# Kernel tuning notes

Hardware: AMD Instinct MI355X
Metric: run time of the kernel (lower is better)

Reference implementation:

```python
import jax, jax.numpy as jnp
import numpy as np
from jax import lax

V, D, H, K, B, T = 32000, 300, 300, 9, 64, 512


def _lstm_dir(x, w_ih, w_hh, b_ih, b_hh, h0, c0):
    # x: [B, T, D]; torch gate order: i, f, g, o
    def step(carry, xt):
        h, c = carry
        gates = xt @ w_ih.T + h @ w_hh.T + b_ih + b_hh  # [B, 4H]
        i, f, g, o = jnp.split(gates, 4, axis=-1)
        i, f, o = jax.nn.sigmoid(i), jax.nn.sigmoid(f), jax.nn.sigmoid(o)
        g = jnp.tanh(g)
        c = f * c + i * g
        h = o * jnp.tanh(c)
        return (h, c), h

    xs = jnp.transpose(x, (1, 0, 2))  # [T, B, D]
    _, hs = lax.scan(step, (h0, c0), xs)
    return jnp.transpose(hs, (1, 0, 2))  # [B, T, H]


def _emissions(tokens, emb, w_ih_f, w_hh_f, b_ih_f, b_hh_f,
               w_ih_b, w_hh_b, b_ih_b, b_hh_b, h0, c0, w_out, b_out):
    x = emb[tokens]  # [B, T, D]
    hf = _lstm_dir(x, w_ih_f, w_hh_f, b_ih_f, b_hh_f, h0[0], c0[0])
    hb = _lstm_dir(jnp.flip(x, axis=1), w_ih_b, w_hh_b, b_ih_b, b_hh_b, h0[1], c0[1])
    hb = jnp.flip(hb, axis=1)
    out = jnp.concatenate([hf, hb], axis=-1)  # [B, T, 2H]
    return out @ w_out.T + b_out  # [B, T, K]


def _crf_nll(emissions, tags, mask, start_t, end_t, trans):
    # torchcrf: -sum_b log p(tags | emissions)
    e = jnp.transpose(emissions, (1, 0, 2))  # [T, B, K]
    tg = tags.T                               # [T, B]
    m = mask.T.astype(emissions.dtype)        # [T, B]
    bidx = jnp.arange(tags.shape[0])
    # numerator: gold path score
    num = start_t[tg[0]] + e[0][bidx, tg[0]]
    def nstep(carry, inp):
        et, tt, tp, mt = inp
        return carry + (trans[tp, tt] + et[bidx, tt]) * mt, None
    num, _ = lax.scan(nstep, num, (e[1:], tg[1:], tg[:-1], m[1:]))
    last_idx = mask.sum(axis=1).astype(jnp.int32) - 1
    last_tags = tags[bidx, last_idx]
    num = num + end_t[last_tags]
    # denominator: forward algorithm
    alpha = start_t + e[0]  # [B, K]
    def dstep(alpha, inp):
        et, mt = inp
        nxt = jax.scipy.special.logsumexp(alpha[:, :, None] + trans[None], axis=1) + et
        return jnp.where(mt[:, None] > 0, nxt, alpha), None
    alpha, _ = lax.scan(dstep, alpha, (e[1:], m[1:]))
    den = jax.scipy.special.logsumexp(alpha + end_t, axis=1)
    return -jnp.sum(num - den)


def _viterbi(emissions, mask, start_t, end_t, trans):
    e = jnp.transpose(emissions, (1, 0, 2))  # [T, B, K]
    m = mask.T                               # [T, B]
    score = start_t + e[0]                   # [B, K]
    def fstep(score, inp):
        et, mt = inp
        br = score[:, :, None] + trans[None]  # [B, K_prev, K_next]
        best = br.max(axis=1)
        idx = br.argmax(axis=1).astype(jnp.int32)  # [B, K]
        new = best + et
        return jnp.where(mt[:, None], new, score), idx
    score, history = lax.scan(fstep, score, (e[1:], m[1:]))  # history: [T-1, B, K]
    score = score + end_t
    last = jnp.argmax(score, axis=-1).astype(jnp.int32)  # [B]
    def bstep(tag, inp):
        idx_t, mt = inp
        prev = jnp.take_along_axis(idx_t, tag[:, None], axis=1)[:, 0]
        tag = jnp.where(mt, prev, tag)
        return tag, tag
    _, tags_rev = lax.scan(bstep, last, (history, m[1:]), reverse=True)  # [T-1, B]
    path = jnp.concatenate([tags_rev, last[None]], axis=0)  # [T, B]
    return path.T  # [B, T]


def setup_inputs() -> dict:
    key = jax.random.key(0)
    ks = jax.random.split(key, 20)
    s = 0.1
    emb = jax.random.normal(ks[0], (V, D), jnp.float32) * s
    emb = emb.at[0].set(0.0)  # padding_idx row
    inp = {
        "tokens": jax.random.randint(ks[1], (B, T), 0, V, jnp.int32),
        "tags": jax.random.randint(ks[2], (B, T), 0, K, jnp.int32),
        "mask": jnp.ones((B, T), jnp.bool_),
        "emb": emb,
        "w_ih_f": jax.random.normal(ks[3], (4 * H, D), jnp.float32) * s,
        "w_hh_f": jax.random.normal(ks[4], (4 * H, H), jnp.float32) * s,
        "b_ih_f": jax.random.normal(ks[5], (4 * H,), jnp.float32) * s,
        "b_hh_f": jax.random.normal(ks[6], (4 * H,), jnp.float32) * s,
        "w_ih_b": jax.random.normal(ks[7], (4 * H, D), jnp.float32) * s,
        "w_hh_b": jax.random.normal(ks[8], (4 * H, H), jnp.float32) * s,
        "b_ih_b": jax.random.normal(ks[9], (4 * H,), jnp.float32) * s,
        "b_hh_b": jax.random.normal(ks[10], (4 * H,), jnp.float32) * s,
        "h0": jax.random.normal(ks[11], (2, B, H), jnp.float32),
        "c0": jax.random.normal(ks[12], (2, B, H), jnp.float32),
        "w_out": jax.random.normal(ks[13], (K, 2 * H), jnp.float32) * s,
        "b_out": jax.random.normal(ks[14], (K,), jnp.float32) * s,
        "start_t": jax.random.normal(ks[15], (K,), jnp.float32) * s,
        "end_t": jax.random.normal(ks[16], (K,), jnp.float32) * s,
        "trans": jax.random.normal(ks[17], (K, K), jnp.float32) * s,
    }
    return inp


def reference(tokens, tags, mask, emb, w_ih_f, w_hh_f, b_ih_f, b_hh_f,
              w_ih_b, w_hh_b, b_ih_b, b_hh_b, h0, c0, w_out, b_out,
              start_t, end_t, trans):
    feats = _emissions(tokens, emb, w_ih_f, w_hh_f, b_ih_f, b_hh_f,
                       w_ih_b, w_hh_b, b_ih_b, b_hh_b, h0, c0, w_out, b_out)
    paths = _viterbi(feats, mask, start_t, end_t, trans)
    loss = _crf_nll(feats, tags, mask, start_t, end_t, trans)
    return paths, loss
```

## Files before the change

kernel.cpp:

```cpp
#include <hip/hip_runtime.h>
#include <math.h>

#define NV 32000
#define ND 300
#define NH 300
#define NK 9
#define NB 64
#define NT 512

typedef short bf16x8 __attribute__((ext_vector_type(8)));
typedef float f32x4  __attribute__((ext_vector_type(4)));

__device__ inline short bf16r(float x) {
    return (short)((__float_as_uint(x) + 0x8000u) >> 16);
}

__device__ inline float tanh_fast(float x) {
    float e2 = __expf(2.f * x);
    return 1.f - 2.f / (e2 + 1.f);
}

__device__ inline void bar_lds() {
    asm volatile("s_waitcnt lgkmcnt(0)" ::: "memory");
    __builtin_amdgcn_s_barrier();
    asm volatile("" ::: "memory");
}

#define WB_OFF   0ull
#define WB_F     768000ull
#define E_OFF    (WB_OFF + WB_F)
#define E_SZ     ((unsigned long long)NT*NB*NK)
#define CBUF_OFF (E_OFF + E_SZ)
#define CBUF_SZ  (2ull*NB*NH)
#define HSLOT_OFF (CBUF_OFF + CBUF_SZ)
#define HSLOT_SZ  (2ull*2*NB*NH)
#define XP_OFF   (HSLOT_OFF + HSLOT_SZ)
#define XPC_SZ   (2ull*64*1200*64)

__global__ __launch_bounds__(256) void k_wcvt(
    const float* __restrict__ wihf, const float* __restrict__ wihb,
    const float* __restrict__ whhf, const float* __restrict__ whhb,
    short* __restrict__ dst)
{
    int i = blockIdx.x*256 + threadIdx.x;
    if (i >= 1536000) return;
    int d  = i / 384000;
    int r2 = i % 384000;
    int j  = r2 / 320, k = r2 % 320;
    const float* src = (d == 0) ? wihf : (d == 1) ? wihb : (d == 2) ? whhf : whhb;
    float v = (k < 300) ? src[(size_t)j*300 + k] : 0.f;
    dst[i] = bf16r(v);
}

__global__ __launch_bounds__(256) void k_xproj(
    const int* __restrict__ tokens, const float* __restrict__ emb,
    const short* __restrict__ wb16,
    const float* __restrict__ bif, const float* __restrict__ bhf,
    const float* __restrict__ bib, const float* __restrict__ bhb,
    float* __restrict__ xpc, int chunk)
{
    const int tid = threadIdx.x;
    const int w  = tid >> 6, L = tid & 63;
    const int lm = L & 15, lq = L >> 4;
    const int dir = blockIdx.z;
    const int m0 = blockIdx.x*128 + w*32;
    const int n0 = blockIdx.y*80;
    const int tbase = dir ? (448 - chunk*64) : (chunk*64);

    const float* arow[2];
#pragma unroll
    for (int mi = 0; mi < 2; ++mi) {
        int m = m0 + mi*16 + lm;
        int b = m >> 6, lt = m & 63;
        arow[mi] = emb + (size_t)tokens[b*512 + tbase + lt] * 300;
    }
    const short* brow[5];
#pragma unroll
    for (int ni = 0; ni < 5; ++ni) {
        int j = n0 + ni*16 + lm;
        brow[ni] = wb16 + ((size_t)dir*1200 + j)*320;
    }

    f32x4 acc[2][5];
#pragma unroll
    for (int mi = 0; mi < 2; ++mi)
#pragma unroll
        for (int ni = 0; ni < 5; ++ni)
#pragma unroll
            for (int r = 0; r < 4; ++r) acc[mi][ni][r] = 0.f;

    const float4 z4 = make_float4(0.f,0.f,0.f,0.f);
    for (int k0 = 0; k0 < 320; k0 += 32) {
        const int kk = k0 + lq*8;
        bf16x8 af[2], bf[5];
#pragma unroll
        for (int mi = 0; mi < 2; ++mi) {
            float4 f1 = (kk   < 300) ? *(const float4*)(arow[mi] + kk)     : z4;
            float4 f2 = (kk+4 < 300) ? *(const float4*)(arow[mi] + kk + 4) : z4;
            af[mi][0]=bf16r(f1.x); af[mi][1]=bf16r(f1.y); af[mi][2]=bf16r(f1.z); af[mi][3]=bf16r(f1.w);
            af[mi][4]=bf16r(f2.x); af[mi][5]=bf16r(f2.y); af[mi][6]=bf16r(f2.z); af[mi][7]=bf16r(f2.w);
        }
#pragma unroll
        for (int ni = 0; ni < 5; ++ni)
            bf[ni] = *(const bf16x8*)(brow[ni] + kk);
#pragma unroll
        for (int mi = 0; mi < 2; ++mi)
#pragma unroll
            for (int ni = 0; ni < 5; ++ni)
                acc[mi][ni] = __builtin_amdgcn_mfma_f32_16x16x32_bf16(
                                  af[mi], bf[ni], acc[mi][ni], 0, 0, 0);
    }

#pragma unroll
    for (int ni = 0; ni < 5; ++ni) {
        int j = n0 + ni*16 + lm;
        int g = j/300, rr = j%300;
        int slc = rr/20, ul = rr%20;
        float bias = dir ? (bib[j]+bhb[j]) : (bif[j]+bhf[j]);
#pragma unroll
        for (int mi = 0; mi < 2; ++mi) {
#pragma unroll
            for (int r = 0; r < 4; ++r) {
                int m = m0 + mi*16 + lq*4 + r;
                int b = m >> 6, lt = m & 63;
                int sp = dir ? (63 - lt) : lt;
                size_t idx = ((((size_t)dir*64 + sp)*8 + (b>>3))*15 + slc)*640
                           + (size_t)(b&7)*80 + g*20 + ul;
                xpc[idx] = acc[mi][ni][r] + bias;
            }
        }
    }
}

__global__ __launch_bounds__(256) void k_rnn(
    const float* __restrict__ xpc,
    const short* __restrict__ whh16,
    const float* __restrict__ h0,
    unsigned* hslot, float* __restrict__ cbuf,
    float* __restrict__ ev, const float* __restrict__ wout,
    int s_begin, int s_count, int full)
{
    extern __shared__ char lds_pad[];
    __shared__ __align__(16) short h_sh16[16*328];
    __shared__ __align__(16) float xp_sh[640];
    __shared__ __align__(16) float gates_sh[80*9];
    __shared__ __align__(16) float wo_sh[180];
    __shared__ __align__(16) float hloc[160];
    __shared__ __align__(16) float ev_loc[64*72];
    (void)lds_pad;

    const int tid = threadIdx.x;
    const int wv  = tid >> 6, L = tid & 63;
    const int lm  = L & 15, lq = L >> 4;
    const int dir = blockIdx.x / 120;
    const int rem = blockIdx.x % 120;
    const int sl  = rem / 8;
    const int gb  = rem % 8;
    const int u0  = sl * 20;

    const int tb = (wv == 0) ? 0 : (wv + 1);
    const int tn = (wv == 0) ? 2 : 1;

    bf16x8 A[2][10];
#pragma unroll 2
    for (int mt = 0; mt < 2; ++mt) {
        if (mt < tn) {
            int r = (tb + mt)*16 + lm;
            int grow = (r/20)*300 + u0 + (r%20);
            const short* wr = whh16 + ((size_t)dir*1200 + grow)*320;
#pragma unroll
            for (int ks = 0; ks < 10; ++ks)
                A[mt][ks] = *(const bf16x8*)(wr + ks*32 + lq*8);
        }
    }
    if (tid < 180) wo_sh[tid] = wout[(tid/20)*600 + dir*300 + u0 + (tid%20)];

    for (int i = tid; i < 16*328; i += 256) h_sh16[i] = 0;

    const bool isPW = (tid < 160);
    const int bl_p = tid/20, lu_p = tid%20;
    float c_reg = 0.f;
    if (isPW) c_reg = cbuf[((size_t)dir*NB + gb*8 + bl_p)*NH + u0 + lu_p];

    auto xaddr = [&](int s) -> const float* {
        const float* xb; int sp;
        if (full) { xb = xpc + (size_t)(s >> 6)*XPC_SZ; sp = s & 63; }
        else      { xb = xpc;                            sp = s - s_begin; }
        return xb + ((((size_t)dir*64 + sp)*8 + gb)*15 + sl)*640 + (size_t)tid*4;
    };
    float4 xpr;
    if (tid < 160) xpr = *(const float4*)xaddr(s_begin);

    bar_lds();

    for (int s = s_begin; s < s_begin + s_count; ++s) {
        unsigned vb[10];
        unsigned* hsrc = hslot + (((size_t)(s & 1)*2 + dir)*NB + gb*8)*NH;
        if (s > 0 && tid < 240) {
#pragma unroll
            for (int j = 0; j < 10; ++j) {
                int i = tid + 256*j;
                if (i < 2400)
                    vb[j] = __hip_atomic_load(hsrc + i, __ATOMIC_RELAXED,
                                              __HIP_MEMORY_SCOPE_AGENT);
            }
        }

        if (tid < 160) *(float4*)(&xp_sh[tid*4]) = xpr;
        if (tid < 160 && (s + 1) < s_begin + s_count)
            xpr = *(const float4*)xaddr(s + 1);

        if (s == 0) {
            const float* h0p = h0 + ((size_t)dir*NB + gb*8)*NH;
            for (int i = tid; i < 2400; i += 256)
                h_sh16[(i/300)*328 + (i%300)] = bf16r(h0p[i]);
        } else if (tid < 240) {
            const unsigned tg = (unsigned)s & 0xFFFFu;
            bool ok = false;
            while (!ok) {
                ok = true;
#pragma unroll
                for (int j = 0; j < 10; ++j) {
                    int i = tid + 256*j;
                    if (i < 2400 && (vb[j] >> 16) != tg) {
                        ok = false;
                        vb[j] = __hip_atomic_load(hsrc + i, __ATOMIC_RELAXED,
                                                  __HIP_MEMORY_SCOPE_AGENT);
                    }
                }
            }
#pragma unroll
            for (int j = 0; j < 10; ++j) {
                int i = tid + 256*j;
                if (i < 2400)
                    h_sh16[(i/300)*328 + (i%300)] = (short)(vb[j] & 0xFFFFu);
            }
        }
        bar_lds();

        {
            bf16x8 Bf[10];
#pragma unroll
            for (int ks = 0; ks < 10; ++ks)
                Bf[ks] = *(const bf16x8*)(h_sh16 + lm*328 + ks*32 + lq*8);
            f32x4 acc0, acc1;
#pragma unroll 2
            for (int mt = 0; mt < 2; ++mt) {
                if (mt < tn) {
#pragma unroll
                    for (int r = 0; r < 4; ++r) { acc0[r] = 0.f; acc1[r] = 0.f; }
#pragma unroll
                    for (int ks = 0; ks < 5; ++ks)
                        acc0 = __builtin_amdgcn_mfma_f32_16x16x32_bf16(
                                   A[mt][ks], Bf[ks], acc0, 0, 0, 0);
#pragma unroll
                    for (int ks = 5; ks < 10; ++ks)
                        acc1 = __builtin_amdgcn_mfma_f32_16x16x32_bf16(
                                   A[mt][ks], Bf[ks], acc1, 0, 0, 0);
                    if (lm < 8) {
#pragma unroll
                        for (int r = 0; r < 4; ++r)
                            gates_sh[((tb+mt)*16 + lq*4 + r)*9 + lm] = acc0[r] + acc1[r];
                    }
                }
            }
        }
        bar_lds();

        if (isPW) {
            float G[4];
#pragma unroll
            for (int g = 0; g < 4; ++g)
                G[g] = xp_sh[bl_p*80 + g*20 + lu_p] + gates_sh[(g*20 + lu_p)*9 + bl_p];
            float ig = 1.f/(1.f+__expf(-G[0]));
            float fg = 1.f/(1.f+__expf(-G[1]));
            float gg = tanh_fast(G[2]);
            float og = 1.f/(1.f+__expf(-G[3]));
            c_reg = fg*c_reg + ig*gg;
            float h = og*tanh_fast(c_reg);
            unsigned hb = (__float_as_uint(h) + 0x8000u) >> 16;
            unsigned pk = (((unsigned)(s+1) & 0xFFFFu) << 16) | hb;
            __hip_atomic_store(
                &hslot[(((size_t)((s+1)&1)*2 + dir)*NB + gb*8 + bl_p)*NH + u0 + lu_p],
                pk, __ATOMIC_RELAXED, __HIP_MEMORY_SCOPE_AGENT);
            hloc[bl_p*20 + lu_p] = h;
        }
        bar_lds();

        const int widx = (s - s_begin) & 63;
        if (tid < 72) {
            int b = tid/9, k = tid%9;
            float a = 0.f;
#pragma unroll
            for (int u = 0; u < 20; ++u) a += hloc[b*20+u]*wo_sh[k*20+u];
            ev_loc[widx*72 + tid] = a;
        }

        if (widx == 63) {
            bar_lds();
            const int sbase = s - 63;
            for (int i = tid; i < 64*72; i += 256) {
                int wi = i / 72, j = i % 72;
                int bb = j / 9, kk = j % 9;
                int tt = dir ? (511 - (sbase + wi)) : (sbase + wi);
                atomicAdd(&ev[((size_t)tt*NB + gb*8 + bb)*NK + kk], ev_loc[i]);
            }
        }
    }

    if (isPW) cbuf[((size_t)dir*NB + gb*8 + bl_p)*NH + u0 + lu_p] = c_reg;
}

#define BT_C 14
#define BT_L 37

__global__ __launch_bounds__(128) void k_crf(
    const float* __restrict__ ev, const int* __restrict__ tags,
    const float* __restrict__ start_t, const float* __restrict__ end_t,
    const float* __restrict__ trans, const float* __restrict__ bout,
    float* __restrict__ out)
{
    __shared__ __align__(16) float ex_a[12];
    __shared__ __align__(16) float ex_v[12];
    __shared__ int hist_sh[511*NK];
    __shared__ int fmap[BT_C*NK];
    __shared__ int entry_sh[BT_C];
    __shared__ int last_sh;

    const int b = blockIdx.x, tid = threadIdx.x;
    const int wv = tid >> 6, ln = tid & 63;

    if (wv == 0) {
        float part = 0.f;
        for (int t = ln; t < NT; t += 64) {
            int tc = tags[b*NT + t];
            float e = ev[((size_t)t*NB + b)*NK + tc] + bout[tc];
            float pre = (t == 0) ? start_t[tc] : trans[tags[b*NT + t - 1]*9 + tc];
            part += pre + e;
        }
        if (ln == 63) part += end_t[tags[b*NT + NT - 1]];
#pragma unroll
        for (int off = 32; off > 0; off >>= 1)
            part += __shfl_down(part, off, 64);
        const float num = part;

        if (ln < 9) {
            const int kc = ln;
            float Tc[9];
#pragma unroll
            for (int kp = 0; kp < 9; ++kp) Tc[kp] = __expf(trans[kp*9 + kc]);
            const float bo = bout[kc];
            ex_a[kc] = start_t[kc] + ev[(size_t)b*NK + kc] + bo;
            float etn = ev[((size_t)1*NB + b)*NK + kc] + bo;

            for (int t = 1; t < NT; ++t) {
                float et = etn;
                if (t + 1 < NT) etn = ev[((size_t)(t+1)*NB + b)*NK + kc] + bo;

                float4 s0 = *(const float4*)(&ex_a[0]);
                float4 s1 = *(const float4*)(&ex_a[4]);
                float  a8 = ex_a[8];
                float a0=s0.x,a1=s0.y,a2=s0.z,a3=s0.w,a4=s1.x,a5=s1.y,a6=s1.z,a7=s1.w;

                float M = fmaxf(fmaxf(fmaxf(a0,a1),fmaxf(a2,a3)),
                                fmaxf(fmaxf(a4,a5),fmaxf(a6,a7)));
                M = fmaxf(M, a8);
                float s =        __expf(a0-M)*Tc[0];
                s = fmaf(__expf(a1-M), Tc[1], s);
                s = fmaf(__expf(a2-M), Tc[2], s);
                s = fmaf(__expf(a3-M), Tc[3], s);
                s = fmaf(__expf(a4-M), Tc[4], s);
                s = fmaf(__expf(a5-M), Tc[5], s);
                s = fmaf(__expf(a6-M), Tc[6], s);
                s = fmaf(__expf(a7-M), Tc[7], s);
                s = fmaf(__expf(a8-M), Tc[8], s);
                ex_a[kc] = M + __logf(s) + et;
            }

            if (ln == 0) {
                float M = -1e30f;
#pragma unroll
                for (int k = 0; k < 9; ++k) M = fmaxf(M, ex_a[k] + end_t[k]);
                float ls = 0.f;
#pragma unroll
                for (int k = 0; k < 9; ++k) ls += __expf(ex_a[k] + end_t[k] - M);
                float den = M + __logf(ls);
                atomicAdd(out + NB*NT, den - num);
            }
        }
    } else {
        if (ln < 9) {
            const int kc = ln;
            float Tc[9];
#pragma unroll
            for (int kp = 0; kp < 9; ++kp) Tc[kp] = trans[kp*9 + kc];
            const float bo = bout[kc];
            ex_v[kc] = start_t[kc] + ev[(size_t)b*NK + kc] + bo;
            float etn = ev[((size_t)1*NB + b)*NK + kc] + bo;

            for (int t = 1; t < NT; ++t) {
                float et = etn;
                if (t + 1 < NT) etn = ev[((size_t)(t+1)*NB + b)*NK + kc] + bo;

                float4 s0 = *(const float4*)(&ex_v[0]);
                float4 s1 = *(const float4*)(&ex_v[4]);
                float  a8 = ex_v[8];
                float a0=s0.x,a1=s0.y,a2=s0.z,a3=s0.w,a4=s1.x,a5=s1.y,a6=s1.z,a7=s1.w;

                float bv = a0 + Tc[0]; int arg = 0;
                float v;
                v = a1+Tc[1]; if (v > bv) { bv = v; arg = 1; }
                v = a2+Tc[2]; if (v > bv) { bv = v; arg = 2; }
                v = a3+Tc[3]; if (v > bv) { bv = v; arg = 3; }
                v = a4+Tc[4]; if (v > bv) { bv = v; arg = 4; }
                v = a5+Tc[5]; if (v > bv) { bv = v; arg = 5; }
                v = a6+Tc[6]; if (v > bv) { bv = v; arg = 6; }
                v = a7+Tc[7]; if (v > bv) { bv = v; arg = 7; }
                v = a8+Tc[8]; if (v > bv) { bv = v; arg = 8; }
                hist_sh[(t-1)*NK + kc] = arg;
                ex_v[kc] = bv + et;
            }

            if (ln == 0) {
                float best = -1e30f; int last = 0;
#pragma unroll
                for (int k = 0; k < 9; ++k) {
                    float v = ex_v[k] + end_t[k];
                    if (v > best) { best = v; last = k; }
                }
                last_sh = last;
            }
        }
    }

    __syncthreads();

    if (tid < BT_C*NK) {
        int c = tid / NK, s = tid % NK;
        int lo = c*BT_L, hi = min(511, lo + BT_L);
        int pos = s;
        for (int i = hi - 1; i >= lo; --i) pos = hist_sh[i*NK + pos];
        fmap[c*NK + s] = pos;
    }
    __syncthreads();
    if (tid == 0) {
        int e = last_sh;
        entry_sh[BT_C-1] = e;
        for (int c = BT_C - 2; c >= 0; --c) {
            e = fmap[(c+1)*NK + e];
            entry_sh[c] = e;
        }
    }
    __syncthreads();
    int* pout = (int*)out;
    if (tid < BT_C) {
        int c = tid;
        int lo = c*BT_L, hi = min(511, lo + BT_L);
        int pos = entry_sh[c];
        for (int i = hi - 1; i >= lo; --i) {
            pos = hist_sh[i*NK + pos];
            pout[b*NT + i] = pos;
        }
    }
    if (tid == 0) pout[b*NT + NT - 1] = last_sh;
}

extern "C" void kernel_launch(void* const* d_in, const int* in_sizes, int n_in,
                              void* d_out, int out_size, void* d_ws, size_t ws_size,
                              hipStream_t stream)
{
    (void)in_sizes; (void)n_in;

    const int*   tokens = (const int*)  d_in[0];
    const int*   tags   = (const int*)  d_in[1];
    const float* emb    = (const float*)d_in[3];
    const float* wihf   = (const float*)d_in[4];
    const float* whhf   = (const float*)d_in[5];
    const float* bihf   = (const float*)d_in[6];
    const float* bhhf   = (const float*)d_in[7];
    const float* wihb   = (const float*)d_in[8];
    const float* whhb   = (const float*)d_in[9];
    const float* bib    = (const float*)d_in[10];
    const float* bhhb   = (const float*)d_in[11];
    const float* h0     = (const float*)d_in[12];
    const float* c0     = (const float*)d_in[13];
    const float* wout   = (const float*)d_in[14];
    const float* bout   = (const float*)d_in[15];
    const float* startt = (const float*)d_in[16];
    const float* endt   = (const float*)d_in[17];
    const float* trans  = (const float*)d_in[18];

    float* ws    = (float*)d_ws;
    short* wb16  = (short*)(ws + WB_OFF);
    short* whh16 = wb16 + 768000;
    float* evp   = ws + E_OFF;
    float* cbuf  = ws + CBUF_OFF;
    unsigned* hslot = (unsigned*)(ws + HSLOT_OFF);
    float* xp    = ws + XP_OFF;
    float* out   = (float*)d_out;

    const size_t need_full = (XP_OFF + 8ull*XPC_SZ) * 4ull;
    const bool full = (ws_size >= need_full);

    (void)hipMemsetAsync(d_out, 0, (size_t)out_size * sizeof(float), stream);
    (void)hipMemsetAsync(evp, 0, (size_t)E_SZ * sizeof(float), stream);
    (void)hipMemcpyAsync(cbuf, c0, 2ull*NB*NH*sizeof(float), hipMemcpyDeviceToDevice, stream);

    k_wcvt<<<6000, 256, 0, stream>>>(wihf, wihb, whhf, whhb, wb16);

    if (full) {
        for (int c = 0; c < 8; ++c)
            k_xproj<<<dim3(32, 15, 2), 256, 0, stream>>>(
                tokens, emb, wb16, bihf, bhhf, bib, bhhb, xp + (size_t)c*XPC_SZ, c);
        k_rnn<<<240, 256, 81920, stream>>>(
            xp, whh16, h0, hslot, cbuf, evp, wout, 0, 512, 1);
    } else {
        for (int c = 0; c < 8; ++c) {
            k_xproj<<<dim3(32, 15, 2), 256, 0, stream>>>(
                tokens, emb, wb16, bihf, bhhf, bib, bhhb, xp, c);
            k_rnn<<<240, 256, 81920, stream>>>(
                xp, whh16, h0, hslot, cbuf, evp, wout, c*64, 64, 0);
        }
    }
    k_crf<<<64, 128, 0, stream>>>(evp, tags, startt, endt, trans, bout, out);
}
```

Before: 2.005 ms.

## Fuse input projection and recurrence into one kernel with chunked software pipelining

Merges the input-projection GEMM and the LSTM recurrence into a single kernel. Blocks 0-239 run the recurrence for a 32-step chunk while the remaining blocks compute the projection for the next chunk into a double buffer. This hides projection work behind the latency-bound recurrence and drops the large full-sequence projection buffer. In exchange there are 17 launches instead of 9, chunks are half as long so more per-chunk setup and launch overhead, and the recurrence blocks share the GPU with GEMM blocks, which can slow their spin-wait synchronization.

```diff
diff --git a/kernel.cpp b/kernel.cpp
--- a/kernel.cpp
+++ b/kernel.cpp
@@ -35,7 +35,7 @@
 #define HSLOT_OFF (CBUF_OFF + CBUF_SZ)
 #define HSLOT_SZ  (2ull*2*NB*NH)
 #define XP_OFF   (HSLOT_OFF + HSLOT_SZ)
-#define XPC_SZ   (2ull*64*1200*64)
+#define XPC32_SZ (2ull*32*1200*64)
 
 __global__ __launch_bounds__(256) void k_wcvt(
     const float* __restrict__ wihf, const float* __restrict__ wihb,
@@ -52,263 +52,264 @@
     dst[i] = bf16r(v);
 }
 
-__global__ __launch_bounds__(256) void k_xproj(
+__global__ __launch_bounds__(256) void k_fused(
     const int* __restrict__ tokens, const float* __restrict__ emb,
     const short* __restrict__ wb16,
     const float* __restrict__ bif, const float* __restrict__ bhf,
     const float* __restrict__ bib, const float* __restrict__ bhb,
-    float* __restrict__ xpc, int chunk)
-{
-    const int tid = threadIdx.x;
-    const int w  = tid >> 6, L = tid & 63;
-    const int lm = L & 15, lq = L >> 4;
-    const int dir = blockIdx.z;
-    const int m0 = blockIdx.x*128 + w*32;
-    const int n0 = blockIdx.y*80;
-    const int tbase = dir ? (448 - chunk*64) : (chunk*64);
-
-    const float* arow[2];
-#pragma unroll
-    for (int mi = 0; mi < 2; ++mi) {
-        int m = m0 + mi*16 + lm;
-        int b = m >> 6, lt = m & 63;
-        arow[mi] = emb + (size_t)tokens[b*512 + tbase + lt] * 300;
-    }
-    const short* brow[5];
-#pragma unroll
-    for (int ni = 0; ni < 5; ++ni) {
-        int j = n0 + ni*16 + lm;
-        brow[ni] = wb16 + ((size_t)dir*1200 + j)*320;
-    }
-
-    f32x4 acc[2][5];
-#pragma unroll
-    for (int mi = 0; mi < 2; ++mi)
-#pragma unroll
-        for (int ni = 0; ni < 5; ++ni)
-#pragma unroll
-            for (int r = 0; r < 4; ++r) acc[mi][ni][r] = 0.f;
-
-    const float4 z4 = make_float4(0.f,0.f,0.f,0.f);
-    for (int k0 = 0; k0 < 320; k0 += 32) {
-        const int kk = k0 + lq*8;
-        bf16x8 af[2], bf[5];
-#pragma unroll
-        for (int mi = 0; mi < 2; ++mi) {
-            float4 f1 = (kk   < 300) ? *(const float4*)(arow[mi] + kk)     : z4;
-            float4 f2 = (kk+4 < 300) ? *(const float4*)(arow[mi] + kk + 4) : z4;
-            af[mi][0]=bf16r(f1.x); af[mi][1]=bf16r(f1.y); af[mi][2]=bf16r(f1.z); af[mi][3]=bf16r(f1.w);
-            af[mi][4]=bf16r(f2.x); af[mi][5]=bf16r(f2.y); af[mi][6]=bf16r(f2.z); af[mi][7]=bf16r(f2.w);
-        }
-#pragma unroll
-        for (int ni = 0; ni < 5; ++ni)
-            bf[ni] = *(const bf16x8*)(brow[ni] + kk);
-#pragma unroll
-        for (int mi = 0; mi < 2; ++mi)
-#pragma unroll
-            for (int ni = 0; ni < 5; ++ni)
-                acc[mi][ni] = __builtin_amdgcn_mfma_f32_16x16x32_bf16(
-                                  af[mi], bf[ni], acc[mi][ni], 0, 0, 0);
-    }
-
-#pragma unroll
-    for (int ni = 0; ni < 5; ++ni) {
-        int j = n0 + ni*16 + lm;
-        int g = j/300, rr = j%300;
-        int slc = rr/20, ul = rr%20;
-        float bias = dir ? (bib[j]+bhb[j]) : (bif[j]+bhf[j]);
-#pragma unroll
-        for (int mi = 0; mi < 2; ++mi) {
-#pragma unroll
-            for (int r = 0; r < 4; ++r) {
-                int m = m0 + mi*16 + lq*4 + r;
-                int b = m >> 6, lt = m & 63;
-                int sp = dir ? (63 - lt) : lt;
-                size_t idx = ((((size_t)dir*64 + sp)*8 + (b>>3))*15 + slc)*640
-                           + (size_t)(b&7)*80 + g*20 + ul;
-                xpc[idx] = acc[mi][ni][r] + bias;
-            }
-        }
-    }
-}
-
-__global__ __launch_bounds__(256) void k_rnn(
-    const float* __restrict__ xpc,
+    float* __restrict__ xp_dst, int chunk_next,
+    const float* __restrict__ xp_src,
     const short* __restrict__ whh16,
     const float* __restrict__ h0,
     unsigned* hslot, float* __restrict__ cbuf,
     float* __restrict__ ev, const float* __restrict__ wout,
-    int s_begin, int s_count, int full)
+    int s_begin, int do_rnn)
 {
-    extern __shared__ char lds_pad[];
     __shared__ __align__(16) short h_sh16[16*328];
     __shared__ __align__(16) float xp_sh[640];
     __shared__ __align__(16) float gates_sh[80*9];
     __shared__ __align__(16) float wo_sh[180];
     __shared__ __align__(16) float hloc[160];
-    __shared__ __align__(16) float ev_loc[64*72];
-    (void)lds_pad;
+    __shared__ __align__(16) float ev_loc[32*72];
 
     const int tid = threadIdx.x;
-    const int wv  = tid >> 6, L = tid & 63;
-    const int lm  = L & 15, lq = L >> 4;
-    const int dir = blockIdx.x / 120;
-    const int rem = blockIdx.x % 120;
-    const int sl  = rem / 8;
-    const int gb  = rem % 8;
-    const int u0  = sl * 20;
-
-    const int tb = (wv == 0) ? 0 : (wv + 1);
-    const int tn = (wv == 0) ? 2 : 1;
-
-    bf16x8 A[2][10];
+    const int nrnn = do_rnn ? 240 : 0;
+
+    if ((int)blockIdx.x < nrnn) {
+        const int wv  = tid >> 6, L = tid & 63;
+        const int lm  = L & 15, lq = L >> 4;
+        const int dir = blockIdx.x / 120;
+        const int rem = blockIdx.x % 120;
+        const int sl  = rem / 8;
+        const int gb  = rem % 8;
+        const int u0  = sl * 20;
+
+        const int tb = (wv == 0) ? 0 : (wv + 1);
+        const int tn = (wv == 0) ? 2 : 1;
+
+        bf16x8 A[2][10];
 #pragma unroll 2
-    for (int mt = 0; mt < 2; ++mt) {
-        if (mt < tn) {
-            int r = (tb + mt)*16 + lm;
-            int grow = (r/20)*300 + u0 + (r%20);
-            const short* wr = whh16 + ((size_t)dir*1200 + grow)*320;
-#pragma unroll
-            for (int ks = 0; ks < 10; ++ks)
-                A[mt][ks] = *(const bf16x8*)(wr + ks*32 + lq*8);
-        }
-    }
-    if (tid < 180) wo_sh[tid] = wout[(tid/20)*600 + dir*300 + u0 + (tid%20)];
-
-    for (int i = tid; i < 16*328; i += 256) h_sh16[i] = 0;
-
-    const bool isPW = (tid < 160);
-    const int bl_p = tid/20, lu_p = tid%20;
-    float c_reg = 0.f;
-    if (isPW) c_reg = cbuf[((size_t)dir*NB + gb*8 + bl_p)*NH + u0 + lu_p];
-
-    auto xaddr = [&](int s) -> const float* {
-        const float* xb; int sp;
-        if (full) { xb = xpc + (size_t)(s >> 6)*XPC_SZ; sp = s & 63; }
-        else      { xb = xpc;                            sp = s - s_begin; }
-        return xb + ((((size_t)dir*64 + sp)*8 + gb)*15 + sl)*640 + (size_t)tid*4;
-    };
-    float4 xpr;
-    if (tid < 160) xpr = *(const float4*)xaddr(s_begin);
-
-    bar_lds();
-
-    for (int s = s_begin; s < s_begin + s_count; ++s) {
-        unsigned vb[10];
-        unsigned* hsrc = hslot + (((size_t)(s & 1)*2 + dir)*NB + gb*8)*NH;
-        if (s > 0 && tid < 240) {
-#pragma unroll
-            for (int j = 0; j < 10; ++j) {
-                int i = tid + 256*j;
-                if (i < 2400)
-                    vb[j] = __hip_atomic_load(hsrc + i, __ATOMIC_RELAXED,
-                                              __HIP_MEMORY_SCOPE_AGENT);
-            }
-        }
-
-        if (tid < 160) *(float4*)(&xp_sh[tid*4]) = xpr;
-        if (tid < 160 && (s + 1) < s_begin + s_count)
-            xpr = *(const float4*)xaddr(s + 1);
-
-        if (s == 0) {
-            const float* h0p = h0 + ((size_t)dir*NB + gb*8)*NH;
-            for (int i = tid; i < 2400; i += 256)
-                h_sh16[(i/300)*328 + (i%300)] = bf16r(h0p[i]);
-        } else if (tid < 240) {
-            const unsigned tg = (unsigned)s & 0xFFFFu;
-            bool ok = false;
-            while (!ok) {
-                ok = true;
+        for (int mt = 0; mt < 2; ++mt) {
+            if (mt < tn) {
+                int r = (tb + mt)*16 + lm;
+                int grow = (r/20)*300 + u0 + (r%20);
+                const short* wr = whh16 + ((size_t)dir*1200 + grow)*320;
+#pragma unroll
+                for (int ks = 0; ks < 10; ++ks)
+                    A[mt][ks] = *(const bf16x8*)(wr + ks*32 + lq*8);
+            }
+        }
+        if (tid < 180) wo_sh[tid] = wout[(tid/20)*600 + dir*300 + u0 + (tid%20)];
+
+        for (int i = tid; i < 16*328; i += 256) h_sh16[i] = 0;
+
+        const bool isPW = (tid < 160);
+        const int bl_p = tid/20, lu_p = tid%20;
+        float c_reg = 0.f;
+        if (isPW) c_reg = cbuf[((size_t)dir*NB + gb*8 + bl_p)*NH + u0 + lu_p];
+
+        auto xaddr = [&](int s) -> const float* {
+            int sp = s - s_begin;
+            return xp_src + ((((size_t)dir*32 + sp)*8 + gb)*15 + sl)*640
+                          + (size_t)tid*4;
+        };
+        float4 xpr;
+        if (tid < 160) xpr = *(const float4*)xaddr(s_begin);
+
+        bar_lds();
+
+        for (int s = s_begin; s < s_begin + 32; ++s) {
+            unsigned vb[10];
+            unsigned* hsrc = hslot + (((size_t)(s & 1)*2 + dir)*NB + gb*8)*NH;
+            if (s > 0 && tid < 240) {
 #pragma unroll
                 for (int j = 0; j < 10; ++j) {
                     int i = tid + 256*j;
-                    if (i < 2400 && (vb[j] >> 16) != tg) {
-                        ok = false;
+                    if (i < 2400)
                         vb[j] = __hip_atomic_load(hsrc + i, __ATOMIC_RELAXED,
                                                   __HIP_MEMORY_SCOPE_AGENT);
+                }
+            }
+
+            if (tid < 160) *(float4*)(&xp_sh[tid*4]) = xpr;
+            if (tid < 160 && (s + 1) < s_begin + 32)
+                xpr = *(const float4*)xaddr(s + 1);
+
+            if (s == 0) {
+                const float* h0p = h0 + ((size_t)dir*NB + gb*8)*NH;
+                for (int i = tid; i < 2400; i += 256)
+                    h_sh16[(i/300)*328 + (i%300)] = bf16r(h0p[i]);
+            } else if (tid < 240) {
+                const unsigned tg = (unsigned)s & 0xFFFFu;
+                bool ok = false;
+                while (!ok) {
+                    ok = true;
+#pragma unroll
+                    for (int j = 0; j < 10; ++j) {
+                        int i = tid + 256*j;
+                        if (i < 2400 && (vb[j] >> 16) != tg) {
+                            ok = false;
+                            vb[j] = __hip_atomic_load(hsrc + i, __ATOMIC_RELAXED,
+                                                      __HIP_MEMORY_SCOPE_AGENT);
+                        }
                     }
                 }
-            }
-#pragma unroll
-            for (int j = 0; j < 10; ++j) {
-                int i = tid + 256*j;
-                if (i < 2400)
-                    h_sh16[(i/300)*328 + (i%300)] = (short)(vb[j] & 0xFFFFu);
-            }
-        }
-        bar_lds();
-
-        {
-            bf16x8 Bf[10];
-#pragma unroll
-            for (int ks = 0; ks < 10; ++ks)
-                Bf[ks] = *(const bf16x8*)(h_sh16 + lm*328 + ks*32 + lq*8);
-            f32x4 acc0, acc1;
+#pragma unroll
+                for (int j = 0; j < 10; ++j) {
+                    int i = tid + 256*j;
+                    if (i < 2400)
+                        h_sh16[(i/300)*328 + (i%300)] = (short)(vb[j] & 0xFFFFu);
+                }
+            }
+            bar_lds();
+
+            {
+                bf16x8 Bf[10];
+#pragma unroll
+                for (int ks = 0; ks < 10; ++ks)
+                    Bf[ks] = *(const bf16x8*)(h_sh16 + lm*328 + ks*32 + lq*8);
+                f32x4 acc0, acc1;
 #pragma unroll 2
-            for (int mt = 0; mt < 2; ++mt) {
-                if (mt < tn) {
-#pragma unroll
-                    for (int r = 0; r < 4; ++r) { acc0[r] = 0.f; acc1[r] = 0.f; }
-#pragma unroll
-                    for (int ks = 0; ks < 5; ++ks)
-                        acc0 = __builtin_amdgcn_mfma_f32_16x16x32_bf16(
-                                   A[mt][ks], Bf[ks], acc0, 0, 0, 0);
-#pragma unroll
-                    for (int ks = 5; ks < 10; ++ks)
-                        acc1 = __builtin_amdgcn_mfma_f32_16x16x32_bf16(
-                                   A[mt][ks], Bf[ks], acc1, 0, 0, 0);
-                    if (lm < 8) {
-#pragma unroll
-                        for (int r = 0; r < 4; ++r)
-                            gates_sh[((tb+mt)*16 + lq*4 + r)*9 + lm] = acc0[r] + acc1[r];
+                for (int mt = 0; mt < 2; ++mt) {
+                    if (mt < tn) {
+#pragma unroll
+                        for (int r = 0; r < 4; ++r) { acc0[r] = 0.f; acc1[r] = 0.f; }
+#pragma unroll
+                        for (int ks = 0; ks < 5; ++ks)
+                            acc0 = __builtin_amdgcn_mfma_f32_16x16x32_bf16(
+                                       A[mt][ks], Bf[ks], acc0, 0, 0, 0);
+#pragma unroll
+                        for (int ks = 5; ks < 10; ++ks)
+                            acc1 = __builtin_amdgcn_mfma_f32_16x16x32_bf16(
+                                       A[mt][ks], Bf[ks], acc1, 0, 0, 0);
+                        if (lm < 8) {
+#pragma unroll
+                            for (int r = 0; r < 4; ++r)
+                                gates_sh[((tb+mt)*16 + lq*4 + r)*9 + lm] = acc0[r] + acc1[r];
+                        }
                     }
                 }
             }
-        }
-        bar_lds();
-
-        if (isPW) {
-            float G[4];
-#pragma unroll
-            for (int g = 0; g < 4; ++g)
-                G[g] = xp_sh[bl_p*80 + g*20 + lu_p] + gates_sh[(g*20 + lu_p)*9 + bl_p];
-            float ig = 1.f/(1.f+__expf(-G[0]));
-            float fg = 1.f/(1.f+__expf(-G[1]));
-            float gg = tanh_fast(G[2]);
-            float og = 1.f/(1.f+__expf(-G[3]));
-            c_reg = fg*c_reg + ig*gg;
-            float h = og*tanh_fast(c_reg);
-            unsigned hb = (__float_as_uint(h) + 0x8000u) >> 16;
-            unsigned pk = (((unsigned)(s+1) & 0xFFFFu) << 16) | hb;
-            __hip_atomic_store(
-                &hslot[(((size_t)((s+1)&1)*2 + dir)*NB + gb*8 + bl_p)*NH + u0 + lu_p],
-                pk, __ATOMIC_RELAXED, __HIP_MEMORY_SCOPE_AGENT);
-            hloc[bl_p*20 + lu_p] = h;
-        }
-        bar_lds();
-
-        const int widx = (s - s_begin) & 63;
-        if (tid < 72) {
-            int b = tid/9, k = tid%9;
-            float a = 0.f;
-#pragma unroll
-            for (int u = 0; u < 20; ++u) a += hloc[b*20+u]*wo_sh[k*20+u];
-            ev_loc[widx*72 + tid] = a;
-        }
-
-        if (widx == 63) {
             bar_lds();
-            const int sbase = s - 63;
-            for (int i = tid; i < 64*72; i += 256) {
-                int wi = i / 72, j = i % 72;
-                int bb = j / 9, kk = j % 9;
-                int tt = dir ? (511 - (sbase + wi)) : (sbase + wi);
-                atomicAdd(&ev[((size_t)tt*NB + gb*8 + bb)*NK + kk], ev_loc[i]);
+
+            if (isPW) {
+                float G[4];
+#pragma unroll
+                for (int g = 0; g < 4; ++g)
+                    G[g] = xp_sh[bl_p*80 + g*20 + lu_p] + gates_sh[(g*20 + lu_p)*9 + bl_p];
+                float ig = 1.f/(1.f+__expf(-G[0]));
+                float fg = 1.f/(1.f+__expf(-G[1]));
+                float gg = tanh_fast(G[2]);
+                float og = 1.f/(1.f+__expf(-G[3]));
+                c_reg = fg*c_reg + ig*gg;
+                float h = og*tanh_fast(c_reg);
+                unsigned hb = (__float_as_uint(h) + 0x8000u) >> 16;
+                unsigned pk = (((unsigned)(s+1) & 0xFFFFu) << 16) | hb;
+                __hip_atomic_store(
+                    &hslot[(((size_t)((s+1)&1)*2 + dir)*NB + gb*8 + bl_p)*NH + u0 + lu_p],
+                    pk, __ATOMIC_RELAXED, __HIP_MEMORY_SCOPE_AGENT);
+                hloc[bl_p*20 + lu_p] = h;
+            }
+            bar_lds();
+
+            const int widx = (s - s_begin) & 31;
+            if (tid < 72) {
+                int b = tid/9, k = tid%9;
+                float a = 0.f;
+#pragma unroll
+                for (int u = 0; u < 20; ++u) a += hloc[b*20+u]*wo_sh[k*20+u];
+                ev_loc[widx*72 + tid] = a;
+            }
+
+            if (widx == 31) {
+                bar_lds();
+                const int sbase = s - 31;
+                for (int i = tid; i < 32*72; i += 256) {
+                    int wi = i / 72, j = i % 72;
+                    int bb = j / 9, kk = j % 9;
+                    int tt = dir ? (511 - (sbase + wi)) : (sbase + wi);
+                    atomicAdd(&ev[((size_t)tt*NB + gb*8 + bb)*NK + kk], ev_loc[i]);
+                }
+            }
+        }
+
+        if (isPW) cbuf[((size_t)dir*NB + gb*8 + bl_p)*NH + u0 + lu_p] = c_reg;
+
+    } else {
+        const int bx = (int)blockIdx.x - nrnn;
+        const int w  = tid >> 6, L = tid & 63;
+        const int lm = L & 15, lq = L >> 4;
+        const int xb = bx & 15;
+        const int yb = (bx >> 4) % 15;
+        const int dir = bx / 240;
+        const int m0 = xb*128 + w*32;
+        const int n0 = yb*80;
+        const int tbase = dir ? (480 - chunk_next*32) : (chunk_next*32);
+
+        const float* arow[2];
+#pragma unroll
+        for (int mi = 0; mi < 2; ++mi) {
+            int m = m0 + mi*16 + lm;
+            int b = m >> 5, lt = m & 31;
+            arow[mi] = emb + (size_t)tokens[b*512 + tbase + lt] * 300;
+        }
+        const short* brow[5];
+#pragma unroll
+        for (int ni = 0; ni < 5; ++ni) {
+            int j = n0 + ni*16 + lm;
+            brow[ni] = wb16 + ((size_t)dir*1200 + j)*320;
+        }
+
+        f32x4 acc[2][5];
+#pragma unroll
+        for (int mi = 0; mi < 2; ++mi)
+#pragma unroll
+            for (int ni = 0; ni < 5; ++ni)
+#pragma unroll
+                for (int r = 0; r < 4; ++r) acc[mi][ni][r] = 0.f;
+
+        const float4 z4 = make_float4(0.f,0.f,0.f,0.f);
+        for (int k0 = 0; k0 < 320; k0 += 32) {
+            const int kk = k0 + lq*8;
+            bf16x8 af[2], bf[5];
+#pragma unroll
+            for (int mi = 0; mi < 2; ++mi) {
+                float4 f1 = (kk   < 300) ? *(const float4*)(arow[mi] + kk)     : z4;
+                float4 f2 = (kk+4 < 300) ? *(const float4*)(arow[mi] + kk + 4) : z4;
+                af[mi][0]=bf16r(f1.x); af[mi][1]=bf16r(f1.y); af[mi][2]=bf16r(f1.z); af[mi][3]=bf16r(f1.w);
+                af[mi][4]=bf16r(f2.x); af[mi][5]=bf16r(f2.y); af[mi][6]=bf16r(f2.z); af[mi][7]=bf16r(f2.w);
+            }
+#pragma unroll
+            for (int ni = 0; ni < 5; ++ni)
+                bf[ni] = *(const bf16x8*)(brow[ni] + kk);
+#pragma unroll
+            for (int mi = 0; mi < 2; ++mi)
+#pragma unroll
+                for (int ni = 0; ni < 5; ++ni)
+                    acc[mi][ni] = __builtin_amdgcn_mfma_f32_16x16x32_bf16(
+                                      af[mi], bf[ni], acc[mi][ni], 0, 0, 0);
+        }
+
+#pragma unroll
+        for (int ni = 0; ni < 5; ++ni) {
+            int j = n0 + ni*16 + lm;
+            int g = j/300, rr = j%300;
+            int slc = rr/20, ul = rr%20;
+            float bias = dir ? (bib[j]+bhb[j]) : (bif[j]+bhf[j]);
+#pragma unroll
+            for (int mi = 0; mi < 2; ++mi) {
+#pragma unroll
+                for (int r = 0; r < 4; ++r) {
+                    int m = m0 + mi*16 + lq*4 + r;
+                    int b = m >> 5, lt = m & 31;
+                    int sp = dir ? (31 - lt) : lt;
+                    size_t idx = ((((size_t)dir*32 + sp)*8 + (b>>3))*15 + slc)*640
+                               + (size_t)(b&7)*80 + g*20 + ul;
+                    xp_dst[idx] = acc[mi][ni][r] + bias;
+                }
             }
         }
     }
-
-    if (isPW) cbuf[((size_t)dir*NB + gb*8 + bl_p)*NH + u0 + lu_p] = c_reg;
 }
 
 #define BT_C 14
@@ -469,7 +470,7 @@
                               void* d_out, int out_size, void* d_ws, size_t ws_size,
                               hipStream_t stream)
 {
-    (void)in_sizes; (void)n_in;
+    (void)in_sizes; (void)n_in; (void)ws_size;
 
     const int*   tokens = (const int*)  d_in[0];
     const int*   tags   = (const int*)  d_in[1];
@@ -499,28 +500,29 @@
     float* xp    = ws + XP_OFF;
     float* out   = (float*)d_out;
 
-    const size_t need_full = (XP_OFF + 8ull*XPC_SZ) * 4ull;
-    const bool full = (ws_size >= need_full);
-
     (void)hipMemsetAsync(d_out, 0, (size_t)out_size * sizeof(float), stream);
     (void)hipMemsetAsync(evp, 0, (size_t)E_SZ * sizeof(float), stream);
     (void)hipMemcpyAsync(cbuf, c0, 2ull*NB*NH*sizeof(float), hipMemcpyDeviceToDevice, stream);
 
     k_wcvt<<<6000, 256, 0, stream>>>(wihf, wihb, whhf, whhb, wb16);
 
-    if (full) {
-        for (int c = 0; c < 8; ++c)
-            k_xproj<<<dim3(32, 15, 2), 256, 0, stream>>>(
-                tokens, emb, wb16, bihf, bhhf, bib, bhhb, xp + (size_t)c*XPC_SZ, c);
-        k_rnn<<<240, 256, 81920, stream>>>(
-            xp, whh16, h0, hslot, cbuf, evp, wout, 0, 512, 1);
-    } else {
-        for (int c = 0; c < 8; ++c) {
-            k_xproj<<<dim3(32, 15, 2), 256, 0, stream>>>(
-                tokens, emb, wb16, bihf, bhhf, bib, bhhb, xp, c);
-            k_rnn<<<240, 256, 81920, stream>>>(
-                xp, whh16, h0, hslot, cbuf, evp, wout, c*64, 64, 0);
-        }
+    k_fused<<<480, 256, 0, stream>>>(
+        tokens, emb, wb16, bihf, bhhf, bib, bhhb,
+        xp, 0,
+        xp, whh16, h0, hslot, cbuf, evp, wout, 0, 0);
+
+    for (int c = 0; c < 15; ++c) {
+        k_fused<<<720, 256, 0, stream>>>(
+            tokens, emb, wb16, bihf, bhhf, bib, bhhb,
+            xp + (size_t)((c+1)&1)*XPC32_SZ, c+1,
+            xp + (size_t)(c&1)*XPC32_SZ, whh16, h0, hslot, cbuf, evp, wout,
+            32*c, 1);
     }
+    k_fused<<<240, 256, 0, stream>>>(
+        tokens, emb, wb16, bihf, bhhf, bib, bhhb,
+        xp, 0,
+        xp + (size_t)XPC32_SZ, whh16, h0, hslot, cbuf, evp, wout,
+        480, 1);
+
     k_crf<<<64, 128, 0, stream>>>(evp, tags, startt, endt, trans, bout, out);
 }
```

Result: faster. 1.930 ms (-3.8%).
